# Kernel optimization log

Measured on AMD Instinct MI355X. Metric: run time of the kernel, lower is better.

The kernel has to match this reference:

```python
import jax, jax.numpy as jnp
import numpy as np

N = 256          # waveguide_dims
ITERN = 3        # iter_num
B = 8192         # batch
INDEX_END = 10   # MNIST classes
ALPHA = 0.1
G = 0.05 * np.pi
PHI_B = np.pi


def setup_inputs() -> dict:
    key = jax.random.key(0)
    k1, k2, k3, k4, k5 = jax.random.split(key, 5)
    two_pi = 2.0 * np.pi
    return {
        "x_real": jax.random.normal(k1, (B, N), dtype=jnp.float32),
        "x_imag": jax.random.normal(k2, (B, N), dtype=jnp.float32),
        "theta": jax.random.uniform(k3, (ITERN, N, N // 2), dtype=jnp.float32) * two_pi,
        "phi":   jax.random.uniform(k4, (ITERN, N, N // 2), dtype=jnp.float32) * two_pi,
        "gamma": jax.random.uniform(k5, (ITERN, N), dtype=jnp.float32) * two_pi,
    }


def _mzi_mesh(x, theta, phi, gamma):
    """Rectangular (Clements) MZI mesh: N layers of 2x2 rotations + output phases.
    x: [B, N] complex64; theta, phi: [N, N//2]; gamma: [N]."""
    L = theta.shape[0]
    shifts = jnp.arange(L) % 2                      # even/odd layer offset
    full = jnp.ones((N // 2,), dtype=bool)
    odd = full.at[-1].set(False)                    # wrap-around pair inactive on odd layers
    masks = jnp.where((shifts == 1)[:, None], odd[None, :], full[None, :])

    def step(xc, inp):
        th, ph, sh, mk = inp
        xr = jnp.roll(xc, -sh, axis=1).reshape(-1, N // 2, 2)
        x0, x1 = xr[..., 0], xr[..., 1]
        half = 0.5 * th
        s, c = jnp.sin(half), jnp.cos(half)
        pre = 1j * jnp.exp(1j * half)               # common MZI prefactor
        ep = jnp.exp(1j * ph)
        y0 = pre * (ep * s * x0 + c * x1)
        y1 = pre * (ep * c * x0 - s * x1)
        y0 = jnp.where(mk, y0, x0)
        y1 = jnp.where(mk, y1, x1)
        y = jnp.stack([y0, y1], axis=-1).reshape(-1, N)
        return jnp.roll(y, sh, axis=1), None

    x, _ = jax.lax.scan(step, x, (theta, phi, shifts, masks))
    return x * jnp.exp(1j * gamma)[None, :]


def _eo_nonlin(x):
    # phase = 0.5*g*|x|^2 + 0.5*phi_b ; out = sqrt(1-alpha)*cos(phase)*exp(-i phase)*x
    phase = 0.5 * G * (x.real ** 2 + x.imag ** 2) + 0.5 * PHI_B
    return np.float32(np.sqrt(1.0 - ALPHA)) * jnp.cos(phase) * jnp.exp(-1j * phase) * x


def reference(x_real, x_imag, theta, phi, gamma):
    x = x_real.astype(jnp.complex64) + 1j * x_imag.astype(jnp.complex64)
    for i in range(ITERN):
        x = _mzi_mesh(x, theta[i], phi[i], gamma[i])
        if i != ITERN - 1:
            x = _eo_nonlin(x)
    intensity = x.real ** 2 + x.imag ** 2            # cnormsq
    norm = jnp.sqrt(jnp.sum(intensity ** 2, axis=1, keepdims=True))
    intensity = intensity / jnp.maximum(norm, 1e-12)  # F.normalize(dim=1)
    return intensity[:, :INDEX_END]
```

## Files before the change

### kernel.cpp

```cpp
#include <hip/hip_runtime.h>
#include <math.h>

#define NWG 256
#define NPAIR 128
#define NITER 3
#define NBATCH 8192
#define KDIM 512
#define MSZ (512*512)

typedef __attribute__((ext_vector_type(8))) short short8;
typedef __attribute__((ext_vector_type(8))) unsigned short ushort8v;
typedef __attribute__((ext_vector_type(4))) float floatx4;

static __device__ __forceinline__ unsigned short f2bf(float f) {
    unsigned int u = __float_as_uint(f);
    unsigned int r = (u + 0x7fffu + ((u >> 16) & 1u)) >> 16;
    return (unsigned short)r;
}
static __device__ __forceinline__ float bf2f(unsigned short h) {
    return __uint_as_float(((unsigned int)h) << 16);
}
static __device__ __forceinline__ void bsplit(float v, unsigned short &h, unsigned short &l) {
    h = f2bf(v);
    l = f2bf(v - bf2f(h));
}
static __device__ __forceinline__ void async16(const void* g, void* l) {
    __builtin_amdgcn_global_load_lds(
        (const __attribute__((address_space(1))) unsigned int*)g,
        (__attribute__((address_space(3))) unsigned int*)l, 16, 0, 0);
}

static __device__ __forceinline__ void apply2(
    float &x0r, float &x0i, float &x1r, float &x1i,
    const float4 a, const float4 b)
{
    float y0r = a.x*x0r - a.y*x0i + a.z*x1r - a.w*x1i;
    float y0i = a.x*x0i + a.y*x0r + a.z*x1i + a.w*x1r;
    float y1r = b.x*x0r - b.y*x0i + b.z*x1r - b.w*x1i;
    float y1i = b.x*x0i + b.y*x0r + b.z*x1i + b.w*x1r;
    x0r = y0r; x0i = y0i; x1r = y1r; x1i = y1i;
}

__global__ void precompute_kernel(const float* __restrict__ theta,
                                  const float* __restrict__ phi,
                                  const float* __restrict__ gamma,
                                  float* __restrict__ coef,
                                  float* __restrict__ coefT,
                                  float* __restrict__ gexp)
{
    int idx = blockIdx.x * blockDim.x + threadIdx.x;
    if (idx < NITER * NWG * NPAIR) {
        float h  = 0.5f * theta[idx];
        float ph = phi[idx];
        float sh = sinf(h),  ch = cosf(h);
        float sp = sinf(ph), cp = cosf(ph);
        float pr = -sh, pii = ch;
        float qr = pr*cp - pii*sp;
        float qi = pr*sp + pii*cp;
        float Ar = qr*sh,  Ai = qi*sh;
        float Br = pr*ch,  Bi = pii*ch;
        float Cr = qr*ch,  Ci = qi*ch;
        float Dr = -pr*sh, Di = -pii*sh;
        float4* o = (float4*)coef + (size_t)idx * 2;
        o[0] = make_float4(Ar,Ai,Br,Bi);
        o[1] = make_float4(Cr,Ci,Dr,Di);
        float4* ot = (float4*)coefT + (size_t)idx * 2;
        ot[0] = make_float4(Ar,Ai,Cr,Ci);
        ot[1] = make_float4(Br,Bi,Dr,Di);
    }
    if (idx < NITER * NWG) {
        float g = gamma[idx];
        gexp[idx*2]   = cosf(g);
        gexp[idx*2+1] = sinf(g);
    }
}

static __device__ __forceinline__ void store_row(
    unsigned short* __restrict__ bh, unsigned short* __restrict__ bl,
    int row, int lane, bool cj, const float xr[4], const float xi[4])
{
    ushort4 reH, reL, imH, imL, nimH, nimL;
    unsigned short h, l;
#pragma unroll
    for (int e = 0; e < 4; ++e) {
        bsplit(xr[e], h, l);  ((unsigned short*)&reH)[e]  = h; ((unsigned short*)&reL)[e]  = l;
        bsplit(xi[e], h, l);  ((unsigned short*)&imH)[e]  = h; ((unsigned short*)&imL)[e]  = l;
        bsplit(-xi[e], h, l); ((unsigned short*)&nimH)[e] = h; ((unsigned short*)&nimL)[e] = l;
    }
    ushort4 urH = cj ? imH : nimH, urL = cj ? imL : nimL;
    ushort4 llH = cj ? nimH : imH, llL = cj ? nimL : imL;
    *(ushort4*)(bh + (size_t)row*KDIM + 4*lane)             = reH;
    *(ushort4*)(bh + (size_t)row*KDIM + 256 + 4*lane)       = urH;
    *(ushort4*)(bh + (size_t)(row+256)*KDIM + 4*lane)       = llH;
    *(ushort4*)(bh + (size_t)(row+256)*KDIM + 256 + 4*lane) = reH;
    *(ushort4*)(bl + (size_t)row*KDIM + 4*lane)             = reL;
    *(ushort4*)(bl + (size_t)row*KDIM + 256 + 4*lane)       = urL;
    *(ushort4*)(bl + (size_t)(row+256)*KDIM + 4*lane)       = llL;
    *(ushort4*)(bl + (size_t)(row+256)*KDIM + 256 + 4*lane) = reL;
}

static __device__ __forceinline__ void layer_compute2(
    const float4 cc[4], int lane, int sp,
    float ar[4], float ai[4], float br[4], float bi[4])
{
    const float4 c0a = cc[0], c0b = cc[1], c1a = cc[2], c1b = cc[3];
    if ((sp & 1) == 0) {
        apply2(ar[0], ai[0], ar[1], ai[1], c0a, c0b);
        apply2(ar[2], ai[2], ar[3], ai[3], c1a, c1b);
        apply2(br[0], bi[0], br[1], bi[1], c0a, c0b);
        apply2(br[2], bi[2], br[3], bi[3], c1a, c1b);
    } else {
        float tAr = __shfl_down(ar[0], 1, 64);
        float tAi = __shfl_down(ai[0], 1, 64);
        float tBr = __shfl_down(br[0], 1, 64);
        float tBi = __shfl_down(bi[0], 1, 64);
        apply2(ar[1], ai[1], ar[2], ai[2], c0a, c0b);
        apply2(br[1], bi[1], br[2], bi[2], c0a, c0b);
        float x3r = ar[3], x3i = ai[3];
        float y3r = c1a.x*x3r - c1a.y*x3i + c1a.z*tAr - c1a.w*tAi;
        float y3i = c1a.x*x3i + c1a.y*x3r + c1a.z*tAi + c1a.w*tAr;
        float ynr = c1b.x*x3r - c1b.y*x3i + c1b.z*tAr - c1b.w*tAi;
        float yni = c1b.x*x3i + c1b.y*x3r + c1b.z*tAi + c1b.w*tAr;
        float w3r = br[3], w3i = bi[3];
        float z3r = c1a.x*w3r - c1a.y*w3i + c1a.z*tBr - c1a.w*tBi;
        float z3i = c1a.x*w3i + c1a.y*w3r + c1a.z*tBi + c1a.w*tBr;
        float znr = c1b.x*w3r - c1b.y*w3i + c1b.z*tBr - c1b.w*tBi;
        float zni = c1b.x*w3i + c1b.y*w3r + c1b.z*tBi + c1b.w*tBr;
        float rAr = __shfl_up(ynr, 1, 64);
        float rAi = __shfl_up(yni, 1, 64);
        float rBr = __shfl_up(znr, 1, 64);
        float rBi = __shfl_up(zni, 1, 64);
        if (lane != 63) { ar[3] = y3r; ai[3] = y3i; br[3] = z3r; bi[3] = z3i; }
        if (lane != 0)  { ar[0] = rAr; ai[0] = rAi; br[0] = rBr; bi[0] = rBi; }
    }
}

__global__ void propagate_kernel(const float* __restrict__ coef,
                                 const float* __restrict__ coefT,
                                 const float* __restrict__ gexp,
                                 unsigned short* __restrict__ chunkH,
                                 unsigned short* __restrict__ chunkL)
{
    __shared__ __align__(16) char smem[3 * 16384];

    const int tid  = threadIdx.x;
    const int lane = tid & 63;
    const int wv   = tid >> 6;
    const int grp  = blockIdx.x >> 6;
    const int it   = grp >> 2, c = grp & 3;
    const int r0   = (blockIdx.x & 63) * 4 + wv * 2;
    const int r1   = r0 + 1;
    const bool rev = (c & 1);
    const bool cj  = (c == 1) || (c == 2);

    float ar[4], ai[4], br[4], bi[4];
    float gc0 = 1.0f, gs0 = 0.0f, gc1 = 1.0f, gs1 = 0.0f;
    if (c == 3) {
        gc0 = gexp[(it*NWG + r0)*2]; gs0 = gexp[(it*NWG + r0)*2 + 1];
        gc1 = gexp[(it*NWG + r1)*2]; gs1 = gexp[(it*NWG + r1)*2 + 1];
    }
#pragma unroll
    for (int e = 0; e < 4; ++e) {
        bool on0 = (4*lane + e) == r0;
        bool on1 = (4*lane + e) == r1;
        ar[e] = on0 ? gc0 : 0.0f;  ai[e] = on0 ? gs0 : 0.0f;
        br[e] = on1 ? gc1 : 0.0f;  bi[e] = on1 ? gs1 : 0.0f;
    }

    const char* cbb = (const char*)(rev ? coefT : coef)
                    + (size_t)(it*NWG + c*64) * (NPAIR * 32);
    const int slot16 = (tid ^ ((tid >> 3) & 3)) * 16;

    auto stage = [&](int m) {
        char* dst = smem + (m % 3) * 16384;
#pragma unroll
        for (int q = 0; q < 4; ++q) {
            int s = 4*m + q;
            int r = rev ? 63 - s : s;
            const char* srow = cbb + (size_t)r * 4096;
            async16(srow + slot16,        dst + q*4096 + tid*16);
            async16(srow + slot16 + 2048, dst + q*4096 + tid*16 + 2048);
        }
    };

    stage(0); stage(1);

    const int sw = (lane >> 1) & 3;
    for (int m = 0; m < 16; ++m) {
        if (m < 15) asm volatile("s_waitcnt vmcnt(8)" ::: "memory");
        else        asm volatile("s_waitcnt vmcnt(0)" ::: "memory");
        __builtin_amdgcn_s_barrier();
        asm volatile("" ::: "memory");
        if (m < 14) stage(m + 2);
        const char* B = smem + (m % 3) * 16384;

        float4 cc[4][4];
#pragma unroll
        for (int q = 0; q < 4; ++q) {
            const char* Bq = B + q*4096;
            cc[q][0] = *(const float4*)(Bq + 16*(4*lane + (0 ^ sw)));
            cc[q][1] = *(const float4*)(Bq + 16*(4*lane + (1 ^ sw)));
            cc[q][2] = *(const float4*)(Bq + 16*(4*lane + (2 ^ sw)));
            cc[q][3] = *(const float4*)(Bq + 16*(4*lane + (3 ^ sw)));
        }
#pragma unroll
        for (int q = 0; q < 4; ++q) {
            int s = 4*m + q;
            layer_compute2(cc[q], lane, rev ? 63 - s : s, ar, ai, br, bi);
        }
    }

    unsigned short* bh = chunkH + (size_t)grp * MSZ;
    unsigned short* bl = chunkL + (size_t)grp * MSZ;
    store_row(bh, bl, r0, lane, cj, ar, ai);
    store_row(bh, bl, r1, lane, cj, br, bi);
}

__global__ __launch_bounds__(256, 2) void compose_kernel(
    const unsigned short* __restrict__ srcH, const unsigned short* __restrict__ srcL,
    unsigned short* __restrict__ outH, unsigned short* __restrict__ outL,
    unsigned short* __restrict__ bmat, int mode)
{
    __shared__ unsigned short sAh[3][2048], sAl[3][2048], sBh[3][2048], sBl[3][2048];
    const int z = blockIdx.z;
    const unsigned short *Ah, *Al, *Bh, *Bl;
    if (mode == 0) {
        int it = z >> 1, wh = z & 1;
        int ai = it*4 + (wh ? 3 : 0), bi = it*4 + (wh ? 2 : 1);
        Ah = srcH + (size_t)ai*MSZ; Al = srcL + (size_t)ai*MSZ;
        Bh = srcH + (size_t)bi*MSZ; Bl = srcL + (size_t)bi*MSZ;
    } else {
        Ah = srcH + (size_t)(2*z+1)*MSZ; Al = srcL + (size_t)(2*z+1)*MSZ;
        Bh = srcH + (size_t)(2*z)*MSZ;   Bl = srcL + (size_t)(2*z)*MSZ;
    }
    const int tid = threadIdx.x, lane = tid & 63, wv = tid >> 6;
    const int quad = lane >> 4, l16 = lane & 15;
    const int m0 = blockIdx.x * 64, n0 = blockIdx.y * 64;
    const unsigned short* src = (wv==0)?Ah:(wv==1)?Al:(wv==2)?Bh:Bl;
    unsigned short (*dstb)[2048] = (wv==0)?sAh:(wv==1)?sAl:(wv==2)?sBh:sBl;
    const int r0 = (wv < 2) ? m0 : n0;
    const int trowb = lane >> 2, tcol = (lane & 3) * 8;

    const unsigned short* sp[4];
#pragma unroll
    for (int i = 0; i < 4; ++i)
        sp[i] = src + (size_t)(r0 + i*16 + trowb)*KDIM + tcol;

    auto stage = [&](int s) {
        int kt = s * 32, bs = s % 3;
#pragma unroll
        for (int i = 0; i < 4; ++i)
            async16(sp[i] + kt, &dstb[bs][i*512 + lane*8]);
    };
    stage(0); stage(1);

    floatx4 acc[4] = {};
    for (int s = 0; s < 16; ++s) {
        if (s < 15) asm volatile("s_waitcnt vmcnt(4)" ::: "memory");
        else        asm volatile("s_waitcnt vmcnt(0)" ::: "memory");
        __builtin_amdgcn_s_barrier();
        asm volatile("" ::: "memory");
        if (s < 14) stage(s + 2);
        const int bs = s % 3;
        short8 ah = *(const short8*)&sAh[bs][(16*wv + l16)*32 + quad*8];
        short8 al = *(const short8*)&sAl[bs][(16*wv + l16)*32 + quad*8];
#pragma unroll
        for (int ni = 0; ni < 4; ++ni) {
            short8 bh = *(const short8*)&sBh[bs][(16*ni + l16)*32 + quad*8];
            short8 bl = *(const short8*)&sBl[bs][(16*ni + l16)*32 + quad*8];
            acc[ni] = __builtin_amdgcn_mfma_f32_16x16x32_bf16(ah, bh, acc[ni], 0,0,0);
            acc[ni] = __builtin_amdgcn_mfma_f32_16x16x32_bf16(ah, bl, acc[ni], 0,0,0);
            acc[ni] = __builtin_amdgcn_mfma_f32_16x16x32_bf16(al, bh, acc[ni], 0,0,0);
        }
    }
#pragma unroll
    for (int ni = 0; ni < 4; ++ni)
#pragma unroll
        for (int rg = 0; rg < 4; ++rg) {
            int r = m0 + 16*wv + quad*4 + rg;
            int cc = n0 + 16*ni + l16;
            float v = acc[ni][rg];
            if (mode == 0) {
                float vs = (((z & 1) == 0) && ((r >= 256) != (cc >= 256))) ? -v : v;
                unsigned short h, l; bsplit(vs, h, l);
                outH[(size_t)z*MSZ + (size_t)r*KDIM + cc] = h;
                outL[(size_t)z*MSZ + (size_t)r*KDIM + cc] = l;
            } else {
                bmat[(size_t)z*MSZ + (size_t)r*KDIM + cc] = f2bf(v);
            }
        }
}

__global__ __launch_bounds__(512, 1) void fused_tail_kernel(
    const unsigned short* __restrict__ Bmat,
    const float* __restrict__ xre, const float* __restrict__ xim,
    float* __restrict__ out)
{
    __shared__ __align__(16) char lds[131072];
    const int tid = threadIdx.x, lane = tid & 63, wv = tid >> 6;
    const int quad = lane >> 4, l16 = lane & 15;
    const int rbase = blockIdx.x * 32;
    const int nb = 32 * wv;

    auto sx = [&](int row, int colByte) -> char* {
        return lds + 98304 + row*1024 + (colByte ^ ((row & 7) << 4));
    };

    {
        float4 v0[4], v1[4]; int xr_[4], xc_[4];
#pragma unroll
        for (int c = 0; c < 4; ++c) {
            int k = tid + c*512;
            int row = k >> 6, rem = k & 63, half = rem >> 5, j8 = (rem & 31) << 3;
            const float* s = (half ? xim : xre) + ((size_t)(rbase + row))*256 + j8;
            v0[c] = *(const float4*)s; v1[c] = *(const float4*)(s + 4);
            xr_[c] = row; xc_[c] = (half*256 + j8)*2;
        }
        asm volatile("s_waitcnt vmcnt(0)" ::: "memory");
#pragma unroll
        for (int c = 0; c < 4; ++c) {
            ushort8v u;
            u[0]=f2bf(v0[c].x); u[1]=f2bf(v0[c].y); u[2]=f2bf(v0[c].z); u[3]=f2bf(v0[c].w);
            u[4]=f2bf(v1[c].x); u[5]=f2bf(v1[c].y); u[6]=f2bf(v1[c].z); u[7]=f2bf(v1[c].w);
            *(ushort8v*)sx(xr_[c], xc_[c]) = u;
        }
    }

    auto stageB = [&](int t) {
        const unsigned short* src = Bmat + ((size_t)(t >> 4))*MSZ + (size_t)(t & 15)*32;
        char* dst = lds + (t % 3)*32768;
#pragma unroll
        for (int c = 0; c < 4; ++c) {
            int slot = tid + c*512, r = slot >> 2, q = slot & 3;
            async16(src + (size_t)r*KDIM + q*8, dst + slot*16);
        }
    };
    stageB(0); stageB(1);
    asm volatile("s_waitcnt lgkmcnt(0)" ::: "memory");

    floatx4 accr[2][2] = {}, acci[2][2] = {};

    for (int t = 0; t < 48; ++t) {
        if (t < 46) asm volatile("s_waitcnt vmcnt(4)" ::: "memory");
        else        asm volatile("s_waitcnt vmcnt(0)" ::: "memory");
        __builtin_amdgcn_s_barrier();
        asm volatile("" ::: "memory");
        if (t < 46) stageB(t + 2);

        if (t == 16 || t == 32) {
#pragma unroll
            for (int f = 0; f < 2; ++f)
#pragma unroll
            for (int nl = 0; nl < 2; ++nl)
#pragma unroll
            for (int rg = 0; rg < 4; ++rg) {
                float yr = accr[f][nl][rg], yi = acci[f][nl][rg];
                float I = yr*yr + yi*yi;
                float ph = 0.078539816339744831f * I + 1.5707963267948966f;
                float sp, cp; __sincosf(ph, &sp, &cp);
                float fm = 0.94868329805051381f * cp;
                int row = 16*f + quad*4 + rg;
                int col = nb + 16*nl + l16;
                *(unsigned short*)sx(row, col*2)       = f2bf(fm*(cp*yr + sp*yi));
                *(unsigned short*)sx(row, col*2 + 512) = f2bf(fm*(cp*yi - sp*yr));
            }
            asm volatile("s_waitcnt lgkmcnt(0)" ::: "memory");
            __builtin_amdgcn_s_barrier();
            asm volatile("" ::: "memory");
#pragma unroll
            for (int f = 0; f < 2; ++f)
#pragma unroll
            for (int nl = 0; nl < 2; ++nl) {
                accr[f][nl] = (floatx4){0.f,0.f,0.f,0.f};
                acci[f][nl] = (floatx4){0.f,0.f,0.f,0.f};
            }
        }

        const int kB = (t & 15) * 64;
        const char* Bb = lds + (t % 3)*32768;
        short8 a0 = *(const short8*)sx(l16,      kB + quad*16);
        short8 a1 = *(const short8*)sx(16 + l16, kB + quad*16);
        short8 br0 = *(const short8*)(Bb + (nb + l16)*64 + quad*16);
        short8 br1 = *(const short8*)(Bb + (nb + 16 + l16)*64 + quad*16);
        short8 bi0 = *(const short8*)(Bb + (256 + nb + l16)*64 + quad*16);
        short8 bi1 = *(const short8*)(Bb + (256 + nb + 16 + l16)*64 + quad*16);
        accr[0][0] = __builtin_amdgcn_mfma_f32_16x16x32_bf16(a0, br0, accr[0][0], 0,0,0);
        accr[0][1] = __builtin_amdgcn_mfma_f32_16x16x32_bf16(a0, br1, accr[0][1], 0,0,0);
        accr[1][0] = __builtin_amdgcn_mfma_f32_16x16x32_bf16(a1, br0, accr[1][0], 0,0,0);
        accr[1][1] = __builtin_amdgcn_mfma_f32_16x16x32_bf16(a1, br1, accr[1][1], 0,0,0);
        acci[0][0] = __builtin_amdgcn_mfma_f32_16x16x32_bf16(a0, bi0, acci[0][0], 0,0,0);
        acci[0][1] = __builtin_amdgcn_mfma_f32_16x16x32_bf16(a0, bi1, acci[0][1], 0,0,0);
        acci[1][0] = __builtin_amdgcn_mfma_f32_16x16x32_bf16(a1, bi0, acci[1][0], 0,0,0);
        acci[1][1] = __builtin_amdgcn_mfma_f32_16x16x32_bf16(a1, bi1, acci[1][1], 0,0,0);
    }

    float I[2][2][4];
    float p[2][4];
#pragma unroll
    for (int f = 0; f < 2; ++f)
#pragma unroll
    for (int rg = 0; rg < 4; ++rg) {
        float s = 0.0f;
#pragma unroll
        for (int nl = 0; nl < 2; ++nl) {
            float yr = accr[f][nl][rg], yi = acci[f][nl][rg];
            float Iv = yr*yr + yi*yi;
            I[f][nl][rg] = Iv;
            s += Iv*Iv;
        }
        p[f][rg] = s;
    }
#pragma unroll
    for (int d = 1; d < 16; d <<= 1) {
#pragma unroll
        for (int f = 0; f < 2; ++f)
#pragma unroll
        for (int rg = 0; rg < 4; ++rg)
            p[f][rg] += __shfl_xor(p[f][rg], d, 64);
    }
    float* scr = (float*)lds;
    if (l16 == 0) {
#pragma unroll
        for (int f = 0; f < 2; ++f)
#pragma unroll
        for (int rg = 0; rg < 4; ++rg)
            scr[wv*32 + 16*f + quad*4 + rg] = p[f][rg];
    }
    asm volatile("s_waitcnt lgkmcnt(0)" ::: "memory");
    __builtin_amdgcn_s_barrier();
    asm volatile("" ::: "memory");
    float* invb = (float*)(lds + 2048);
    if (tid < 32) {
        float s = 0.0f;
#pragma unroll
        for (int w = 0; w < 8; ++w) s += scr[w*32 + tid];
        invb[tid] = 1.0f / fmaxf(sqrtf(s), 1e-12f);
    }
    asm volatile("s_waitcnt lgkmcnt(0)" ::: "memory");
    __builtin_amdgcn_s_barrier();
    asm volatile("" ::: "memory");
    if (wv == 0 && l16 < 10) {
#pragma unroll
        for (int f = 0; f < 2; ++f)
#pragma unroll
        for (int rg = 0; rg < 4; ++rg) {
            int row = 16*f + quad*4 + rg;
            out[((size_t)(rbase + row))*10 + l16] = I[f][0][rg] * invb[row];
        }
    }
}

extern "C" void kernel_launch(void* const* d_in, const int* in_sizes, int n_in,
                              void* d_out, int out_size, void* d_ws, size_t ws_size,
                              hipStream_t stream)
{
    const float* x_real = (const float*)d_in[0];
    const float* x_imag = (const float*)d_in[1];
    const float* theta  = (const float*)d_in[2];
    const float* phi    = (const float*)d_in[3];
    const float* gamma  = (const float*)d_in[4];

    char* ws = (char*)d_ws;
    float* coef  = (float*)(ws + 0);
    float* coefT = (float*)(ws + 3145728);
    float* gexp  = (float*)(ws + 6291456);
    unsigned short* chunkH = (unsigned short*)(ws + 6297600);
    unsigned short* chunkL = (unsigned short*)(ws + 12589056);
    unsigned short* PH   = (unsigned short*)(ws + 0);
    unsigned short* PL   = (unsigned short*)(ws + 3145728);
    unsigned short* Bmat = (unsigned short*)(ws + 23074816);

    precompute_kernel<<<(NITER*NWG*NPAIR + 255)/256, 256, 0, stream>>>(
        theta, phi, gamma, coef, coefT, gexp);

    propagate_kernel<<<768, 128, 0, stream>>>(coef, coefT, gexp, chunkH, chunkL);

    compose_kernel<<<dim3(8,8,6), 256, 0, stream>>>(chunkH, chunkL, PH, PL, Bmat, 0);
    compose_kernel<<<dim3(8,8,3), 256, 0, stream>>>(PH, PL, PH, PL, Bmat, 1);

    fused_tail_kernel<<<256, 512, 0, stream>>>(Bmat, x_real, x_imag, (float*)d_out);
}
```

Measured before the change: 157.5 us.

## Split MZI mesh into eight chunks per iteration and add a composition round

The propagate kernel now builds eight 32-layer transfer-matrix chunks per iteration instead of four 64-layer chunks, doubling its grid and halving each block's serial layer chain. A third compose_kernel round is added to multiply the extra chunks together with per-round operand selection and conjugate sign handling, and the workspace is re-laid out to hold the intermediate products. This shortens the serial propagate step in exchange for an extra GEMM launch and more intermediate memory traffic.

```diff
diff --git a/kernel.cpp b/kernel.cpp
--- a/kernel.cpp
+++ b/kernel.cpp
@@ -147,15 +147,15 @@
     const int lane = tid & 63;
     const int wv   = tid >> 6;
     const int grp  = blockIdx.x >> 6;
-    const int it   = grp >> 2, c = grp & 3;
+    const int it   = grp >> 3, c = grp & 7;
     const int r0   = (blockIdx.x & 63) * 4 + wv * 2;
     const int r1   = r0 + 1;
     const bool rev = (c & 1);
-    const bool cj  = (c == 1) || (c == 2);
+    const bool cj  = ((c & 3) == 1) || ((c & 3) == 2);
 
     float ar[4], ai[4], br[4], bi[4];
     float gc0 = 1.0f, gs0 = 0.0f, gc1 = 1.0f, gs1 = 0.0f;
-    if (c == 3) {
+    if (c == 7) {
         gc0 = gexp[(it*NWG + r0)*2]; gs0 = gexp[(it*NWG + r0)*2 + 1];
         gc1 = gexp[(it*NWG + r1)*2]; gs1 = gexp[(it*NWG + r1)*2 + 1];
     }
@@ -168,7 +168,7 @@
     }
 
     const char* cbb = (const char*)(rev ? coefT : coef)
-                    + (size_t)(it*NWG + c*64) * (NPAIR * 32);
+                    + (size_t)(it*NWG + c*32) * (NPAIR * 32);
     const int slot16 = (tid ^ ((tid >> 3) & 3)) * 16;
 
     auto stage = [&](int m) {
@@ -176,7 +176,7 @@
 #pragma unroll
         for (int q = 0; q < 4; ++q) {
             int s = 4*m + q;
-            int r = rev ? 63 - s : s;
+            int r = rev ? 31 - s : s;
             const char* srow = cbb + (size_t)r * 4096;
             async16(srow + slot16,        dst + q*4096 + tid*16);
             async16(srow + slot16 + 2048, dst + q*4096 + tid*16 + 2048);
@@ -186,12 +186,12 @@
     stage(0); stage(1);
 
     const int sw = (lane >> 1) & 3;
-    for (int m = 0; m < 16; ++m) {
-        if (m < 15) asm volatile("s_waitcnt vmcnt(8)" ::: "memory");
-        else        asm volatile("s_waitcnt vmcnt(0)" ::: "memory");
+    for (int m = 0; m < 8; ++m) {
+        if (m < 7) asm volatile("s_waitcnt vmcnt(8)" ::: "memory");
+        else       asm volatile("s_waitcnt vmcnt(0)" ::: "memory");
         __builtin_amdgcn_s_barrier();
         asm volatile("" ::: "memory");
-        if (m < 14) stage(m + 2);
+        if (m < 6) stage(m + 2);
         const char* B = smem + (m % 3) * 16384;
 
         float4 cc[4][4];
@@ -206,7 +206,7 @@
 #pragma unroll
         for (int q = 0; q < 4; ++q) {
             int s = 4*m + q;
-            layer_compute2(cc[q], lane, rev ? 63 - s : s, ar, ai, br, bi);
+            layer_compute2(cc[q], lane, rev ? 31 - s : s, ar, ai, br, bi);
         }
     }
 
@@ -219,16 +219,25 @@
 __global__ __launch_bounds__(256, 2) void compose_kernel(
     const unsigned short* __restrict__ srcH, const unsigned short* __restrict__ srcL,
     unsigned short* __restrict__ outH, unsigned short* __restrict__ outL,
-    unsigned short* __restrict__ bmat, int mode)
+    unsigned short* __restrict__ bmat, int round)
 {
     __shared__ unsigned short sAh[3][2048], sAl[3][2048], sBh[3][2048], sBl[3][2048];
     const int z = blockIdx.z;
     const unsigned short *Ah, *Al, *Bh, *Bl;
-    if (mode == 0) {
-        int it = z >> 1, wh = z & 1;
-        int ai = it*4 + (wh ? 3 : 0), bi = it*4 + (wh ? 2 : 1);
-        Ah = srcH + (size_t)ai*MSZ; Al = srcL + (size_t)ai*MSZ;
-        Bh = srcH + (size_t)bi*MSZ; Bl = srcL + (size_t)bi*MSZ;
+    bool conjOut = false;
+    if (round == 1) {
+        const int aoff[4] = {0, 3, 4, 7}, boff[4] = {1, 2, 5, 6};
+        int w = z & 3, it = z >> 2;
+        int ac = it*8 + aoff[w], bc = it*8 + boff[w];
+        conjOut = (w == 1) || (w == 2);
+        Ah = srcH + (size_t)ac*MSZ; Al = srcL + (size_t)ac*MSZ;
+        Bh = srcH + (size_t)bc*MSZ; Bl = srcL + (size_t)bc*MSZ;
+    } else if (round == 2) {
+        int w = z & 1, it = z >> 1;
+        int ac = it*4 + (w ? 3 : 0), bc = it*4 + (w ? 2 : 1);
+        conjOut = (w == 0);
+        Ah = srcH + (size_t)ac*MSZ; Al = srcL + (size_t)ac*MSZ;
+        Bh = srcH + (size_t)bc*MSZ; Bl = srcL + (size_t)bc*MSZ;
     } else {
         Ah = srcH + (size_t)(2*z+1)*MSZ; Al = srcL + (size_t)(2*z+1)*MSZ;
         Bh = srcH + (size_t)(2*z)*MSZ;   Bl = srcL + (size_t)(2*z)*MSZ;
@@ -280,8 +289,8 @@
             int r = m0 + 16*wv + quad*4 + rg;
             int cc = n0 + 16*ni + l16;
             float v = acc[ni][rg];
-            if (mode == 0) {
-                float vs = (((z & 1) == 0) && ((r >= 256) != (cc >= 256))) ? -v : v;
+            if (round <= 2) {
+                float vs = (conjOut && ((r >= 256) != (cc >= 256))) ? -v : v;
                 unsigned short h, l; bsplit(vs, h, l);
                 outH[(size_t)z*MSZ + (size_t)r*KDIM + cc] = h;
                 outL[(size_t)z*MSZ + (size_t)r*KDIM + cc] = l;
@@ -465,18 +474,22 @@
     float* coefT = (float*)(ws + 3145728);
     float* gexp  = (float*)(ws + 6291456);
     unsigned short* chunkH = (unsigned short*)(ws + 6297600);
-    unsigned short* chunkL = (unsigned short*)(ws + 12589056);
-    unsigned short* PH   = (unsigned short*)(ws + 0);
-    unsigned short* PL   = (unsigned short*)(ws + 3145728);
-    unsigned short* Bmat = (unsigned short*)(ws + 23074816);
+    unsigned short* chunkL = (unsigned short*)(ws + 18880512);
+    unsigned short* R1H = (unsigned short*)(ws + 31463424);
+    unsigned short* R1L = (unsigned short*)(ws + 37754880);
+    unsigned short* R2H = (unsigned short*)(ws + 44046336);
+    unsigned short* R2L = (unsigned short*)(ws + 47192064);
+    unsigned short* Bmat = (unsigned short*)(ws + 50337792);
 
     precompute_kernel<<<(NITER*NWG*NPAIR + 255)/256, 256, 0, stream>>>(
         theta, phi, gamma, coef, coefT, gexp);
 
-    propagate_kernel<<<768, 128, 0, stream>>>(coef, coefT, gexp, chunkH, chunkL);
-
-    compose_kernel<<<dim3(8,8,6), 256, 0, stream>>>(chunkH, chunkL, PH, PL, Bmat, 0);
-    compose_kernel<<<dim3(8,8,3), 256, 0, stream>>>(PH, PL, PH, PL, Bmat, 1);
+    propagate_kernel<<<1536, 128, 0, stream>>>(coef, coefT, gexp, chunkH, chunkL);
+
+    compose_kernel<<<dim3(8,8,12), 256, 0, stream>>>(chunkH, chunkL, R1H, R1L, Bmat, 1);
+    compose_kernel<<<dim3(8,8,6),  256, 0, stream>>>(R1H, R1L, R2H, R2L, Bmat, 2);
+    compose_kernel<<<dim3(8,8,3),  256, 0, stream>>>(R2H, R2L, (unsigned short*)nullptr,
+                                                     (unsigned short*)nullptr, Bmat, 3);
 
     fused_tail_kernel<<<256, 512, 0, stream>>>(Bmat, x_real, x_imag, (float*)d_out);
 }
```

Result: slower. 182.1 us (+15.6%).
